# Performance work log

Hardware: AMD Instinct MI355X
Metric: run time of the kernel (lower is better)

The kernel has to match this reference:

```python
import jax, jax.numpy as jnp
import numpy as np

B, N, Q, H = 32, 1024, 64, 768


def setup_inputs() -> dict:
    key = jax.random.key(0)
    k1, k2, k3, k4 = jax.random.split(key, 4)
    return {
        "nodes_compress": jax.random.normal(k1, (B, N, H), dtype=jnp.float32),
        "query_compress": jax.random.normal(k2, (B, Q, H), dtype=jnp.float32),
        "nodes_hidden": jax.random.normal(k3, (B, N, H), dtype=jnp.float32),
        # nn.Linear(3H, 1, bias=False).weight flattened to (3H,)
        "w": jax.random.normal(k4, (3 * H,), dtype=jnp.float32) * (1.0 / np.sqrt(3 * H)),
    }


def reference(nodes_compress, query_compress, nodes_hidden, w):
    h = nodes_compress.shape[-1]
    w_n, w_q, w_nq = w[:h], w[h:2 * h], w[2 * h:]
    # Decomposed trilinear similarity: identical to Linear([n, q, n*q]) -> scalar
    sim = (
        (nodes_compress @ w_n)[:, :, None]          # (B, N, 1)
        + (query_compress @ w_q)[:, None, :]        # (B, 1, Q)
        + jnp.einsum("bnh,bqh,h->bnq", nodes_compress, query_compress, w_nq)
    )                                                # (B, N, Q)
    # nodes -> query attention
    a = jax.nn.softmax(sim, axis=-1)                 # (B, N, Q)
    nodes2query = jnp.einsum("bnq,bqh->bnh", a, query_compress)
    # query -> nodes attention (max over query, softmax over nodes)
    b = jax.nn.softmax(jnp.max(sim, axis=-1), axis=-1)  # (B, N)
    q2n = jnp.einsum("bn,bnh->bh", b, nodes_compress)[:, None, :]  # (B, 1, H)
    q2n = jnp.broadcast_to(q2n, nodes_compress.shape)               # (B, N, H)
    return jnp.concatenate(
        [nodes_compress, nodes2query, nodes_compress * nodes2query, nodes_compress * q2n],
        axis=-1,
    )  # (B, N, 4H)
```

## Files before the change

kernel.cpp:

```cpp
#include <hip/hip_runtime.h>
#include <hip/hip_bf16.h>

#define BB 32
#define NN 1024
#define QQ 64
#define HH 768

typedef __attribute__((ext_vector_type(8))) short short8;
typedef __attribute__((ext_vector_type(4))) float f32x4;

#define GLOAD_LDS16(gp, lp) \
  __builtin_amdgcn_global_load_lds((const __attribute__((address_space(1))) unsigned int*)(gp), \
                                   (__attribute__((address_space(3))) unsigned int*)(lp), 16, 0, 0)

__device__ __forceinline__ unsigned short f2b(float f) {
  unsigned int u = __float_as_uint(f);
  unsigned int r = u + 0x7fffu + ((u >> 16) & 1u);
  return (unsigned short)(r >> 16);
}

__global__ void k_prep(const float* __restrict__ qc, const float* __restrict__ w,
                       unsigned short* __restrict__ qwB, unsigned short* __restrict__ qcT,
                       float* __restrict__ sq) {
  const int bid = blockIdx.x, tid = threadIdx.x;
  if (bid < 768) {
    int gid = bid * 256 + tid;
    int b = gid / 6144, rem = gid % 6144;
    int q = rem / 96, kk = rem % 96;
    int kc = kk >> 4, uu = kk & 15;
    const float* src = qc + ((size_t)(b * 64 + q) * HH + kk * 8);
    float4 g0 = *(const float4*)src, g1 = *(const float4*)(src + 4);
    int h = kk * 8;
    float4 n0 = *(const float4*)(w + h), n1 = *(const float4*)(w + h + 4);
    float4 m0 = *(const float4*)(w + 2 * HH + h), m1 = *(const float4*)(w + 2 * HH + h + 4);
    short8 v;
    v[0] = (short)f2b(g0.x * m0.x + n0.x); v[1] = (short)f2b(g0.y * m0.y + n0.y);
    v[2] = (short)f2b(g0.z * m0.z + n0.z); v[3] = (short)f2b(g0.w * m0.w + n0.w);
    v[4] = (short)f2b(g1.x * m1.x + n1.x); v[5] = (short)f2b(g1.y * m1.y + n1.y);
    v[6] = (short)f2b(g1.z * m1.z + n1.z); v[7] = (short)f2b(g1.w * m1.w + n1.w);
    size_t du = (size_t)(b * 6 + kc) * 1024 + q * 16 + (uu ^ (q & 7));
    *(short8*)((char*)qwB + du * 16) = v;
  } else if (bid < 1536) {
    int gid = (bid - 768) * 256 + tid;
    int b = gid / 6144, p = gid % 6144;
    int hc = p >> 10, pr = p & 1023, r = pr >> 3, x = pr & 7;
    int xu = x ^ (r & 7);
    int h = hc * 128 + r;
    const float* col = qc + ((size_t)(b * 64 + xu * 8) * HH + h);
    short8 v;
#pragma unroll
    for (int j = 0; j < 8; ++j) v[j] = (short)f2b(col[(size_t)j * HH]);
    *(short8*)((char*)qcT + (size_t)gid * 16) = v;
  } else {
    int wid = ((bid - 1536) * 256 + tid) >> 6;
    int l = tid & 63;
    const float* row = qc + (size_t)wid * HH;
    float s = 0.f;
#pragma unroll
    for (int i = 0; i < 12; ++i) s += row[i * 64 + l] * w[HH + i * 64 + l];
#pragma unroll
    for (int m = 1; m < 64; m <<= 1) s += __shfl_xor(s, m);
    if (l == 0) sq[wid] = s;
  }
}

__global__ __launch_bounds__(256) void k_sim(
    const float* __restrict__ nc, const unsigned short* __restrict__ qwB,
    const float* __restrict__ sq, float* __restrict__ partial,
    float* __restrict__ mtse, unsigned short* __restrict__ probs)
{
  __shared__ __align__(16) char bbuf[2][16384];
  __shared__ float rowmF[64];
  __shared__ float wvF[64];

  const int tid = threadIdx.x;
  const int wv_ = tid >> 6, l = tid & 63;
  const int l15 = l & 15, lg = l >> 4;
  const int b = blockIdx.x >> 4, tile = blockIdx.x & 15;
  const int row0 = tile * 64;

  const float* ncB = nc + (size_t)(b * NN + row0) * HH;
  const char* qwb = (const char*)qwB + (size_t)b * 98304;
  const float* aBase = ncB + (wv_ * 16 + l15) * HH + lg * 8;

  {
    const char* gsrc = qwb + wv_ * 4096 + l * 16;
#pragma unroll
    for (int i = 0; i < 4; ++i)
      GLOAD_LDS16(gsrc + i * 1024, &bbuf[0][wv_ * 4096 + i * 1024]);
  }
  float4 fr[2][8];
#pragma unroll
  for (int ks = 0; ks < 4; ++ks) {
    fr[0][ks * 2]     = *(const float4*)(aBase + ks * 32);
    fr[0][ks * 2 + 1] = *(const float4*)(aBase + ks * 32 + 4);
  }

  f32x4 acc[4] = {};
#pragma unroll
  for (int kc = 0; kc < 6; ++kc) {
    short8 af[4];
#pragma unroll
    for (int ks = 0; ks < 4; ++ks) {
      float4 f0 = fr[kc & 1][ks * 2], f1 = fr[kc & 1][ks * 2 + 1];
      short8 v;
      v[0] = (short)f2b(f0.x); v[1] = (short)f2b(f0.y);
      v[2] = (short)f2b(f0.z); v[3] = (short)f2b(f0.w);
      v[4] = (short)f2b(f1.x); v[5] = (short)f2b(f1.y);
      v[6] = (short)f2b(f1.z); v[7] = (short)f2b(f1.w);
      af[ks] = v;
    }
    if (kc < 5) {
#pragma unroll
      for (int ks = 0; ks < 4; ++ks) {
        fr[(kc + 1) & 1][ks * 2]     = *(const float4*)(aBase + (kc + 1) * 128 + ks * 32);
        fr[(kc + 1) & 1][ks * 2 + 1] = *(const float4*)(aBase + (kc + 1) * 128 + ks * 32 + 4);
      }
      const char* gsrc = qwb + (kc + 1) * 16384 + wv_ * 4096 + l * 16;
#pragma unroll
      for (int i = 0; i < 4; ++i)
        GLOAD_LDS16(gsrc + i * 1024, &bbuf[(kc + 1) & 1][wv_ * 4096 + i * 1024]);
      asm volatile("s_waitcnt vmcnt(12)" ::: "memory");
    } else {
      asm volatile("s_waitcnt vmcnt(0)" ::: "memory");
    }
    __builtin_amdgcn_s_barrier();
    __builtin_amdgcn_sched_barrier(0);
#pragma unroll
    for (int ks = 0; ks < 4; ++ks) {
      int kbyte = ks * 64 + lg * 16;
#pragma unroll
      for (int nt = 0; nt < 4; ++nt) {
        int brow = nt * 16 + l15;
        short8 bf = *(short8*)(&bbuf[kc & 1][0] + brow * 256 + (kbyte ^ ((l & 7) << 4)));
        acc[nt] = __builtin_amdgcn_mfma_f32_16x16x32_bf16(af[ks], bf, acc[nt], 0, 0, 0);
      }
    }
    __builtin_amdgcn_sched_barrier(0);
    __builtin_amdgcn_s_barrier();
  }

  unsigned short* pT = probs + (size_t)(b * 16 + tile) * (QQ * QQ);
  float sqv[4];
#pragma unroll
  for (int nt = 0; nt < 4; ++nt) sqv[nt] = sq[b * QQ + nt * 16 + l15];
#pragma unroll
  for (int j = 0; j < 4; ++j) {
    float mm = -1e30f;
#pragma unroll
    for (int nt = 0; nt < 4; ++nt) { acc[nt][j] += sqv[nt]; mm = fmaxf(mm, acc[nt][j]); }
    mm = fmaxf(mm, __shfl_xor(mm, 1));
    mm = fmaxf(mm, __shfl_xor(mm, 2));
    mm = fmaxf(mm, __shfl_xor(mm, 4));
    mm = fmaxf(mm, __shfl_xor(mm, 8));
    float ss = 0.f;
#pragma unroll
    for (int nt = 0; nt < 4; ++nt) { float p = __expf(acc[nt][j] - mm); acc[nt][j] = p; ss += p; }
    ss += __shfl_xor(ss, 1); ss += __shfl_xor(ss, 2);
    ss += __shfl_xor(ss, 4); ss += __shfl_xor(ss, 8);
    float inv = 1.0f / ss;
    int r = wv_ * 16 + lg * 4 + j;
#pragma unroll
    for (int nt = 0; nt < 4; ++nt)
      pT[r * 64 + nt * 16 + l15] = f2b(acc[nt][j] * inv);
    if (l15 == 0) rowmF[r] = mm;
  }
  __syncthreads();

  float m_t = -1e30f;
#pragma unroll
  for (int i = 0; i < 16; ++i) {
    f32x4 v = ((f32x4*)rowmF)[i];
    m_t = fmaxf(m_t, fmaxf(fmaxf(v[0], v[1]), fmaxf(v[2], v[3])));
  }
  if (tid < 64) wvF[tid] = __expf(rowmF[tid] - m_t);
  __syncthreads();
  {
    float sv = wvF[l];
#pragma unroll
    for (int m = 1; m < 64; m <<= 1) sv += __shfl_xor(sv, m);
    if (tid == 0) {
      mtse[(b * 16 + tile) * 2] = m_t;
      mtse[(b * 16 + tile) * 2 + 1] = sv;
    }
  }
  {
    float p0 = 0.f, p1 = 0.f, p2 = 0.f;
    for (int n = 0; n < 64; ++n) {
      float wvv = wvF[n];
      const float* pr = ncB + n * HH + tid;
      p0 += wvv * pr[0]; p1 += wvv * pr[256]; p2 += wvv * pr[512];
    }
    float* pp = partial + (size_t)(b * 16 + tile) * HH + tid;
    pp[0] = p0; pp[256] = p1; pp[512] = p2;
  }
}

__global__ __launch_bounds__(256) void k_out(
    const float* __restrict__ nc, const unsigned short* __restrict__ qcT,
    const unsigned short* __restrict__ probs, const float* __restrict__ partial,
    const float* __restrict__ mtse, float* __restrict__ out)
{
  __shared__ __align__(16) char smem[16384];
  __shared__ float q2nL[128];

  const int tid = threadIdx.x;
  const int wv_ = tid >> 6, l = tid & 63;
  const int l15 = l & 15, lg = l >> 4;
  const int bid = blockIdx.x;
  const int hc = bid % 6;
  const int bt = bid / 6;
  const int b = bt >> 4, tile = bt & 15;
  const int row0 = tile * 64;

  {
    const char* src = (const char*)qcT + ((size_t)(b * 6 + hc) << 14) + wv_ * 4096 + l * 16;
#pragma unroll
    for (int i = 0; i < 4; ++i)
      GLOAD_LDS16(src + i * 1024, &smem[wv_ * 4096 + i * 1024]);
  }

  if (tid < 128) {
    float M = -1e30f, mt[16], se[16];
#pragma unroll
    for (int i = 0; i < 16; ++i) {
      mt[i] = mtse[(b * 16 + i) * 2];
      se[i] = mtse[(b * 16 + i) * 2 + 1];
      M = fmaxf(M, mt[i]);
    }
    float denom = 0.f;
#pragma unroll
    for (int i = 0; i < 16; ++i) { mt[i] = __expf(mt[i] - M); denom += mt[i] * se[i]; }
    float inv = 1.0f / denom;
    float a = 0.f;
#pragma unroll
    for (int i = 0; i < 16; ++i)
      a += mt[i] * partial[(size_t)(b * 16 + i) * HH + hc * 128 + tid];
    q2nL[tid] = a * inv;
  }

  const unsigned short* pT = probs + (size_t)bt * (QQ * QQ);
  short8 a2_0 = *(const short8*)((const char*)pT + (wv_ * 16 + l15) * 128 + lg * 16);
  short8 a2_1 = *(const short8*)((const char*)pT + (wv_ * 16 + l15) * 128 + 64 + lg * 16);

  asm volatile("s_waitcnt vmcnt(0)" ::: "memory");
  __syncthreads();

  const int n = wv_ * 16 + l15;
  const float* ncrow = nc + (size_t)(b * NN + row0 + n) * HH;
  float* orow = out + (size_t)(b * NN + row0 + n) * 3072;

#pragma unroll
  for (int hg = 0; hg < 8; ++hg) {
    f32x4 c2 = {};
#pragma unroll
    for (int ks2 = 0; ks2 < 2; ++ks2) {
      int hrow = hg * 16 + l15;
      int kbyte = ks2 * 64 + lg * 16;
      short8 hf = *(short8*)(&smem[0] + hrow * 128 + (kbyte ^ ((l & 7) << 4)));
      c2 = __builtin_amdgcn_mfma_f32_16x16x32_bf16(hf, ks2 ? a2_1 : a2_0, c2, 0, 0, 0);
    }
    int hl = hg * 16 + lg * 4;
    int hbase = hc * 128 + hl;
    f32x4 ncv = *(const f32x4*)(ncrow + hbase);
    f32x4 qv  = *(const f32x4*)(&q2nL[hl]);
    *(f32x4*)(orow + hbase)          = ncv;
    *(f32x4*)(orow + HH + hbase)     = c2;
    *(f32x4*)(orow + 2 * HH + hbase) = ncv * c2;
    *(f32x4*)(orow + 2304 + hbase)   = ncv * qv;
  }
}

extern "C" void kernel_launch(void* const* d_in, const int* in_sizes, int n_in,
                              void* d_out, int out_size, void* d_ws, size_t ws_size,
                              hipStream_t stream) {
  (void)in_sizes; (void)n_in; (void)out_size; (void)ws_size;
  const float* nc = (const float*)d_in[0];
  const float* qc = (const float*)d_in[1];
  const float* w  = (const float*)d_in[3];
  float* out = (float*)d_out;
  char* ws = (char*)d_ws;
  unsigned short* qwB = (unsigned short*)(ws);
  unsigned short* qcT = (unsigned short*)(ws + 3145728);
  float* sqv     = (float*)(ws + 6291456);
  float* partial = (float*)(ws + 6299648);
  float* mtse    = (float*)(ws + 7872512);
  unsigned short* probs = (unsigned short*)(ws + 7876608);

  k_prep<<<2048, 256, 0, stream>>>(qc, w, qwB, qcT, sqv);
  k_sim<<<512, 256, 0, stream>>>(nc, qwB, sqv, partial, mtse, probs);
  k_out<<<3072, 256, 0, stream>>>(nc, qcT, probs, partial, mtse, out);
}
```

Measured before the change: 170.1 us.

## Remap block indices for XCD locality and split the q2n partial sum across waves

Both kernels now permute blockIdx so that consecutive logical blocks are spread across the 8 XCDs (blockIdx&7 selects a chunk), keeping blocks of the same batch on the same XCD to improve L2 reuse of shared per-batch data. In k_sim, the weighted partial sum over the 64 node rows is split so that each wave handles 16 rows and 12 columns per lane, followed by an LDS reduction across waves. Previously every thread looped over all 64 rows serially. The change adds 12 KB of LDS and an extra barrier, which may reduce occupancy.

```diff
diff --git a/kernel.cpp b/kernel.cpp
--- a/kernel.cpp
+++ b/kernel.cpp
@@ -72,11 +72,13 @@
   __shared__ __align__(16) char bbuf[2][16384];
   __shared__ float rowmF[64];
   __shared__ float wvF[64];
+  __shared__ float pW[4][768];
 
   const int tid = threadIdx.x;
   const int wv_ = tid >> 6, l = tid & 63;
   const int l15 = l & 15, lg = l >> 4;
-  const int b = blockIdx.x >> 4, tile = blockIdx.x & 15;
+  const int lb = (blockIdx.x & 7) * 64 + (blockIdx.x >> 3);
+  const int b = lb >> 4, tile = lb & 15;
   const int row0 = tile * 64;
 
   const float* ncB = nc + (size_t)(b * NN + row0) * HH;
@@ -185,14 +187,25 @@
     }
   }
   {
-    float p0 = 0.f, p1 = 0.f, p2 = 0.f;
-    for (int n = 0; n < 64; ++n) {
+    float a[12];
+#pragma unroll
+    for (int j = 0; j < 12; ++j) a[j] = 0.f;
+    for (int n0 = 0; n0 < 16; ++n0) {
+      int n = wv_ * 16 + n0;
       float wvv = wvF[n];
-      const float* pr = ncB + n * HH + tid;
-      p0 += wvv * pr[0]; p1 += wvv * pr[256]; p2 += wvv * pr[512];
-    }
+      const float* pr = ncB + (size_t)n * HH;
+#pragma unroll
+      for (int j = 0; j < 12; ++j) a[j] += wvv * pr[l + j * 64];
+    }
+#pragma unroll
+    for (int j = 0; j < 12; ++j) pW[wv_][l + j * 64] = a[j];
+  }
+  __syncthreads();
+  {
     float* pp = partial + (size_t)(b * 16 + tile) * HH + tid;
-    pp[0] = p0; pp[256] = p1; pp[512] = p2;
+    pp[0]   = pW[0][tid]       + pW[1][tid]       + pW[2][tid]       + pW[3][tid];
+    pp[256] = pW[0][tid + 256] + pW[1][tid + 256] + pW[2][tid + 256] + pW[3][tid + 256];
+    pp[512] = pW[0][tid + 512] + pW[1][tid + 512] + pW[2][tid + 512] + pW[3][tid + 512];
   }
 }
 
@@ -207,9 +220,9 @@
   const int tid = threadIdx.x;
   const int wv_ = tid >> 6, l = tid & 63;
   const int l15 = l & 15, lg = l >> 4;
-  const int bid = blockIdx.x;
-  const int hc = bid % 6;
-  const int bt = bid / 6;
+  const int lb = (blockIdx.x & 7) * 384 + (blockIdx.x >> 3);
+  const int hc = lb % 6;
+  const int bt = lb / 6;
   const int b = bt >> 4, tile = bt & 15;
   const int row0 = tile * 64;
 
```

Measured after the change: 157.4 us. -7.5%, faster.
